# Optimization experiments

Hardware: AMD Instinct MI355X
Metric: run time of the kernel (lower is better)

## Reference

```python
import jax, jax.numpy as jnp
import numpy as np

N = 50000   # nodes per side
H = 256     # hidden_dim
E = 800000  # edges per metapath (avg degree 16)
XAVIER_STD = 0.088  # gain 1.414 * sqrt(2/(H+H))


def setup_inputs() -> dict:
    key = jax.random.key(0)
    ks = jax.random.split(key, 32)
    inp = {}
    inp["h_d"] = jax.random.normal(ks[0], (N, H), dtype=jnp.float32)
    inp["h_p"] = jax.random.normal(ks[1], (N, H), dtype=jnp.float32)
    i = 2
    for name in ["d0", "d1", "p0", "p1"]:
        inp[name + "_idx"] = jax.random.randint(ks[i], (2, E), 0, N, dtype=jnp.int32); i += 1
        inp[name + "_val"] = jax.random.uniform(ks[i], (E,), dtype=jnp.float32); i += 1
    # per-metapath GCN params: Linear weight [H,H] (no bias), additive bias [H], PReLU slope (scalar)
    for name in ["d0", "d1", "p0", "p1"]:
        inp["W" + name] = jax.random.normal(ks[i], (H, H), dtype=jnp.float32) * XAVIER_STD; i += 1
        inp["b" + name] = jnp.zeros((H,), jnp.float32)
        inp["a" + name] = jnp.full((1,), 0.25, jnp.float32)
    # per-side attention params: fc weight/bias, att vector [1,H]
    for s in ["d", "p"]:
        inp["fcW" + s] = jax.random.normal(ks[i], (H, H), dtype=jnp.float32) * XAVIER_STD; i += 1
        inp["fcb" + s] = jnp.zeros((H,), jnp.float32)
        inp["att" + s] = jax.random.normal(ks[i], (1, H), dtype=jnp.float32) * XAVIER_STD; i += 1
    return inp


def _gcn(h, W, b, a, idx, val):
    # Linear (no bias) -> sparse COO spmm -> bias -> PReLU
    fts = h @ W.T                                  # [N,H]
    msg = val[:, None] * fts[idx[1]]               # gather source rows [E,H]
    out = jax.ops.segment_sum(msg, idx[0], num_segments=h.shape[0]) + b
    return jnp.where(out > 0, out, a * out)        # PReLU, shared slope


def _attn_fuse(embeds, Wf, bf, att):
    # score_p = att . mean_n(tanh(fc(embed_p)))  -> softmax over metapaths
    sp = jnp.stack([jnp.tanh(e @ Wf.T + bf).mean(axis=0) for e in embeds])  # [P,H]
    beta = jax.nn.softmax(sp @ att[0])                                      # [P]
    return jnp.einsum('p,pnh->nh', beta, jnp.stack(embeds))


def reference(h_d, h_p, d0_idx, d0_val, d1_idx, d1_val, p0_idx, p0_val,
              p1_idx, p1_val, Wd0, bd0, ad0, Wd1, bd1, ad1,
              Wp0, bp0, ap0, Wp1, bp1, ap1,
              fcWd, fcbd, attd, fcWp, fcbp, attp):
    embeds_d = [_gcn(h_d, Wd0, bd0, ad0, d0_idx, d0_val),
                _gcn(h_d, Wd1, bd1, ad1, d1_idx, d1_val)]
    z_d = _attn_fuse(embeds_d, fcWd, fcbd, attd)
    embeds_p = [_gcn(h_p, Wp0, bp0, ap0, p0_idx, p0_val),
                _gcn(h_p, Wp1, bp1, ap1, p1_idx, p1_val)]
    z_p = _attn_fuse(embeds_p, fcWp, fcbp, attp)
    return (z_d, z_p)
```

## Files before the change

kernel.cpp:

```cpp
#include <hip/hip_runtime.h>
#include <cstdint>

#define H 256
#define NBMAX 400
#define CAPB 16

typedef unsigned short u16;
typedef __attribute__((ext_vector_type(8))) short short8;
typedef __attribute__((ext_vector_type(4))) float f32x4;

__device__ __forceinline__ float bf2f(u16 u) {
  return __uint_as_float(((unsigned)u) << 16);
}
__device__ __forceinline__ u16 f2bf(float f) {
  unsigned u = __float_as_uint(f);
  u = (u + 0x7FFF + ((u >> 16) & 1)) >> 16;
  return (u16)u;
}
__device__ __forceinline__ void async16(const void* g, void* l) {
  __builtin_amdgcn_global_load_lds((const __attribute__((address_space(1))) void*)g,
                                   (__attribute__((address_space(3))) void*)l, 16, 0, 0);
}

__global__ __launch_bounds__(256) void cvt_bf16(
    const float* __restrict__ h0, const float* __restrict__ h1,
    u16* __restrict__ dst, int total, size_t NH)
{
  const float* src = blockIdx.y ? h1 : h0;
  u16* d = dst + (size_t)blockIdx.y * NH;
  int i = (blockIdx.x * 256 + threadIdx.x) * 4;
  if (i >= total) return;
  float4 x = *(const float4*)(src + i);
  *(ushort4*)(d + i) = make_ushort4(f2bf(x.x), f2bf(x.y), f2bf(x.z), f2bf(x.w));
}

__global__ __launch_bounds__(256) void cvt_weights(
    const float* w0, const float* w1, const float* w2, const float* w3,
    const float* w4, const float* w5, u16* __restrict__ dst)
{
  const float* srcs[6] = {w0, w1, w2, w3, w4, w5};
  const float* s = srcs[blockIdx.y];
  int i = (blockIdx.x * 256 + threadIdx.x) * 4;
  float4 x = *(const float4*)(s + i);
  *(ushort4*)(dst + blockIdx.y * (H * H) + i) =
      make_ushort4(f2bf(x.x), f2bf(x.y), f2bf(x.z), f2bf(x.w));
}

__device__ __forceinline__ int block_incl_scan(int v) {
  __shared__ int wsum[4];
  int tid = threadIdx.x, lane = tid & 63, w = tid >> 6;
  int x = v;
  #pragma unroll
  for (int off = 1; off < 64; off <<= 1) {
    int n = __shfl_up(x, off);
    if (lane >= off) x += n;
  }
  if (lane == 63) wsum[w] = x;
  __syncthreads();
  int add = 0;
  #pragma unroll
  for (int i = 0; i < 4; ++i) add += (i < w) ? wsum[i] : 0;
  return x + add;
}

__global__ __launch_bounds__(1024) void hist_coarse(
    const int* i0, const int* i1, const int* i2, const int* i3,
    int* __restrict__ bcnt, int E, int nbuck)
{
  int mp = blockIdx.y;
  const int* idxs[4] = {i0, i1, i2, i3};
  const int* idx = idxs[mp];
  __shared__ int lh[NBMAX];
  int t = threadIdx.x;
  for (int i = t; i < nbuck; i += 1024) lh[i] = 0;
  __syncthreads();
  for (int e = blockIdx.x * 1024 + t; e < E; e += gridDim.x * 1024)
    atomicAdd(&lh[idx[e] >> 7], 1);
  __syncthreads();
  for (int i = t; i < nbuck; i += 1024) {
    int v = lh[i];
    if (v) atomicAdd(&bcnt[mp * nbuck + i], v);
  }
}

__global__ __launch_bounds__(256) void scan_buckets(
    const int* __restrict__ bcnt, int* __restrict__ bbase,
    int* __restrict__ gcur, int* __restrict__ rowptr, int N, int E, int nbuck)
{
  int mp = blockIdx.y;
  int t = threadIdx.x;
  int i0 = t * 2, i1 = t * 2 + 1;
  int a = (i0 < nbuck) ? bcnt[mp * nbuck + i0] : 0;
  int b = (i1 < nbuck) ? bcnt[mp * nbuck + i1] : 0;
  int s = a + b;
  int incl = block_incl_scan(s);
  int ex = incl - s;
  if (i0 < nbuck) { bbase[mp * nbuck + i0] = ex;     gcur[mp * nbuck + i0] = ex; }
  if (i1 < nbuck) { bbase[mp * nbuck + i1] = ex + a; gcur[mp * nbuck + i1] = ex + a; }
  if (t == 0) rowptr[mp * (N + 1) + N] = E;
}

__global__ __launch_bounds__(1024) void scatter_binned(
    const int* i0, const int* i1, const int* i2, const int* i3,
    const float* v0, const float* v1, const float* v2, const float* v3,
    int* __restrict__ gcur, int2* __restrict__ edgesB, int E, int nbuck)
{
  int mp = blockIdx.y;
  const int* idxs[4] = {i0, i1, i2, i3};
  const float* vals[4] = {v0, v1, v2, v3};
  const int* idx = idxs[mp];
  const float* val = vals[mp];
  int* cur = gcur + mp * nbuck;
  int2* out = edgesB + (size_t)mp * E;

  __shared__ int cnt[NBMAX];
  __shared__ int2 slab[NBMAX * CAPB];
  int t = threadIdx.x;
  for (int i = t; i < nbuck; i += 1024) cnt[i] = 0;
  __syncthreads();

  for (int base_e = blockIdx.x * 2048; base_e < E; base_e += gridDim.x * 2048) {
    #pragma unroll
    for (int u = 0; u < 2; ++u) {
      int e = base_e + u * 1024 + t;
      if (e < E) {
        int d = idx[e];
        int s = idx[E + e];
        float v = val[e];
        int bb = d >> 7;
        int2 pk = make_int2(s | ((d & 127) << 16), __float_as_int(v));
        int slot = atomicAdd(&cnt[bb], 1);
        if (slot < CAPB) slab[bb * CAPB + slot] = pk;
        else {
          int pos = atomicAdd(&cur[bb], 1);
          out[pos] = pk;
        }
      }
    }
    __syncthreads();
    for (int bb = t; bb < nbuck; bb += 1024) {
      int c = cnt[bb];
      if (c > CAPB) c = CAPB;
      if (c >= 8) {
        int ng = c >> 3;
        int pos = atomicAdd(&cur[bb], ng * 8);
        for (int k = 0; k < ng * 8; ++k) out[pos + k] = slab[bb * CAPB + k];
        int r = c & 7;
        for (int k = 0; k < r; ++k)
          slab[bb * CAPB + k] = slab[bb * CAPB + ng * 8 + k];
        cnt[bb] = r;
      }
    }
    __syncthreads();
  }
  for (int bb = t; bb < nbuck; bb += 1024) {
    int c = cnt[bb];
    if (c > CAPB) c = CAPB;
    if (c > 0) {
      int pos = atomicAdd(&cur[bb], c);
      for (int k = 0; k < c; ++k) out[pos + k] = slab[bb * CAPB + k];
    }
  }
}

__global__ __launch_bounds__(256) void bucket_to_csr(
    const int2* __restrict__ edgesB, const int* __restrict__ bbase,
    int* __restrict__ rowptr, int2* __restrict__ edges, int N, int E, int nbuck)
{
  int mp = blockIdx.y;
  int b = blockIdx.x;
  int base = bbase[mp * nbuck + b];
  int endp = (b + 1 < nbuck) ? bbase[mp * nbuck + b + 1] : E;
  int cntE = endp - base;
  const int2* in = edgesB + (size_t)mp * E + base;
  int2* out = edges + (size_t)mp * E;

  __shared__ int h[128], csum[128];
  int t = threadIdx.x;
  if (t < 128) h[t] = 0;
  __syncthreads();
  for (int k = t; k < cntE; k += 256)
    atomicAdd(&h[(in[k].x >> 16) & 127], 1);
  __syncthreads();
  if (t == 0) {
    int acc = 0;
    for (int i = 0; i < 128; ++i) { int c = h[i]; csum[i] = acc; acc += c; }
  }
  __syncthreads();
  int d0 = b << 7;
  if (t < 128 && d0 + t < N) rowptr[mp * (N + 1) + d0 + t] = base + csum[t];
  if (t < 128) h[t] = csum[t];
  __syncthreads();
  for (int k = t; k < cntE; k += 256) {
    int2 pk = in[k];
    int dl = (pk.x >> 16) & 127;
    int pos = atomicAdd(&h[dl], 1);
    out[base + pos] = make_int2(pk.x & 0xFFFF, pk.y);
  }
}

__global__ __launch_bounds__(256) void spmm_csr(
    const u16* __restrict__ hbf, const int* __restrict__ rowptrAll,
    const int2* __restrict__ edgesAll, u16* __restrict__ aggAll,
    int N, int E, size_t NH)
{
  int mp = blockIdx.y;
  const u16* fts = hbf + (size_t)(mp >> 1) * NH;
  const int* rowptr = rowptrAll + (size_t)mp * (N + 1);
  const int2* edges = edgesAll + (size_t)mp * E;
  u16* agg = aggAll + (size_t)mp * NH;

  int gw = (int)((blockIdx.x * 256 + threadIdx.x) >> 6);
  if (gw >= N) return;
  int lane = threadIdx.x & 63;
  int beg = rowptr[gw], end = rowptr[gw + 1];
  float a0 = 0.f, a1 = 0.f, a2 = 0.f, a3 = 0.f;
  for (int base = beg; base < end; base += 64) {
    int k = base + lane;
    int2 ev = make_int2(0, 0);
    if (k < end) ev = edges[k];
    int cnt = min(64, end - base);
    int j = 0;
    for (; j + 8 <= cnt; j += 8) {
      int sj[8]; float vj[8]; ushort4 r[8];
      #pragma unroll
      for (int u = 0; u < 8; ++u) {
        sj[u] = __shfl(ev.x, j + u);
        vj[u] = __uint_as_float((unsigned)__shfl(ev.y, j + u));
      }
      #pragma unroll
      for (int u = 0; u < 8; ++u)
        r[u] = *(const ushort4*)(fts + (size_t)sj[u] * H + lane * 4);
      #pragma unroll
      for (int u = 0; u < 8; ++u) {
        a0 += vj[u] * bf2f(r[u].x);
        a1 += vj[u] * bf2f(r[u].y);
        a2 += vj[u] * bf2f(r[u].z);
        a3 += vj[u] * bf2f(r[u].w);
      }
    }
    for (; j + 4 <= cnt; j += 4) {
      int sj[4]; float vj[4]; ushort4 r[4];
      #pragma unroll
      for (int u = 0; u < 4; ++u) {
        sj[u] = __shfl(ev.x, j + u);
        vj[u] = __uint_as_float((unsigned)__shfl(ev.y, j + u));
      }
      #pragma unroll
      for (int u = 0; u < 4; ++u)
        r[u] = *(const ushort4*)(fts + (size_t)sj[u] * H + lane * 4);
      #pragma unroll
      for (int u = 0; u < 4; ++u) {
        a0 += vj[u] * bf2f(r[u].x);
        a1 += vj[u] * bf2f(r[u].y);
        a2 += vj[u] * bf2f(r[u].z);
        a3 += vj[u] * bf2f(r[u].w);
      }
    }
    for (; j < cnt; ++j) {
      int sj = __shfl(ev.x, j);
      float vj = __uint_as_float((unsigned)__shfl(ev.y, j));
      ushort4 r = *(const ushort4*)(fts + (size_t)sj * H + lane * 4);
      a0 += vj * bf2f(r.x);
      a1 += vj * bf2f(r.y);
      a2 += vj * bf2f(r.z);
      a3 += vj * bf2f(r.w);
    }
  }
  int c = lane * 4;
  *(ushort4*)(agg + (size_t)gw * H + c) =
      make_ushort4(f2bf(a0), f2bf(a1), f2bf(a2), f2bf(a3));
}

template <int MODE>
__global__ __launch_bounds__(256) void gemm_bt(
    const u16* __restrict__ Abase, const u16* __restrict__ Wbase,
    u16* __restrict__ Cbase,
    const float* bp0, const float* bp1, const float* bp2, const float* bp3,
    const float* ap0, const float* ap1, const float* ap2, const float* ap3,
    float* __restrict__ colsum, int M, size_t NH)
{
  const int pi = blockIdx.z;
  const float* bps[4] = {bp0, bp1, bp2, bp3};
  const float* aps[4] = {ap0, ap1, ap2, ap3};
  const u16* A = Abase + (size_t)pi * NH;
  const u16* W;
  u16* C = nullptr;
  const float* bias;
  float* cs = nullptr;
  float al = 0.f;
  if (MODE == 0) {
    W = Wbase + (size_t)pi * (H * H);
    C = Cbase + (size_t)pi * NH;
    bias = bps[pi];
    al = aps[pi][0];
  } else {
    W = Wbase + (size_t)(pi >> 1) * (H * H);
    bias = (pi >> 1) ? bp1 : bp0;
    cs = colsum + (size_t)pi * H;
  }

  __shared__ u16 As[128 * 64];
  __shared__ u16 Bs[128 * 64];
  const int tid  = threadIdx.x;
  const int lane = tid & 63;
  const int wave = tid >> 6;
  const int quad = lane >> 4;
  const int l15  = lane & 15;
  const int m0 = blockIdx.x * 128;
  const int n0 = blockIdx.y * 128;
  const int wr = (wave & 1) * 64;
  const int wc = (wave >> 1) * 64;

  f32x4 acc[4][4] = {};

  for (int k0 = 0; k0 < H; k0 += 64) {
    #pragma unroll
    for (int r = 0; r < 4; ++r) {
      int chunk = r * 256 + tid;
      int row = chunk >> 3;
      int col = (chunk & 7) * 8;
      int gm = m0 + row; if (gm >= M) gm = M - 1;
      u16* lbase = As + (r * 256 + wave * 64) * 8;
      async16(A + (size_t)gm * H + k0 + col, lbase);
      u16* lbase2 = Bs + (r * 256 + wave * 64) * 8;
      async16(W + (size_t)(n0 + row) * H + k0 + col, lbase2);
    }
    __syncthreads();
    #pragma unroll
    for (int kk = 0; kk < 64; kk += 32) {
      short8 af[4], bf[4];
      #pragma unroll
      for (int i = 0; i < 4; ++i) {
        af[i] = *(const short8*)(As + (wr + i * 16 + l15) * 64 + kk + quad * 8);
        bf[i] = *(const short8*)(Bs + (wc + i * 16 + l15) * 64 + kk + quad * 8);
      }
      #pragma unroll
      for (int mi = 0; mi < 4; ++mi)
        #pragma unroll
        for (int ni = 0; ni < 4; ++ni)
          acc[mi][ni] = __builtin_amdgcn_mfma_f32_16x16x32_bf16(af[mi], bf[ni], acc[mi][ni], 0, 0, 0);
    }
    __syncthreads();
  }

  if (MODE == 0) {
    #pragma unroll
    for (int mi = 0; mi < 4; ++mi)
      #pragma unroll
      for (int ni = 0; ni < 4; ++ni) {
        int n = n0 + wc + ni * 16 + l15;
        float bv = bias[n];
        #pragma unroll
        for (int j = 0; j < 4; ++j) {
          int m = m0 + wr + mi * 16 + quad * 4 + j;
          if (m < M) {
            float x = acc[mi][ni][j] + bv;
            x = x > 0.f ? x : al * x;
            C[(size_t)m * H + n] = f2bf(x);
          }
        }
      }
  } else {
    #pragma unroll
    for (int ni = 0; ni < 4; ++ni) {
      int n = n0 + wc + ni * 16 + l15;
      float bv = bias[n];
      float s = 0.f;
      #pragma unroll
      for (int mi = 0; mi < 4; ++mi)
        #pragma unroll
        for (int j = 0; j < 4; ++j) {
          int m = m0 + wr + mi * 16 + quad * 4 + j;
          if (m < M) {
            float x = acc[mi][ni][j] + bv;
            s += 1.f - 2.f / (__expf(2.f * x) + 1.f);
          }
        }
      s += __shfl_xor(s, 16);
      s += __shfl_xor(s, 32);
      if (lane < 16) unsafeAtomicAdd(&cs[n], s);
    }
  }
}

__global__ __launch_bounds__(256) void compute_beta(
    const float* __restrict__ sp, const float* attd, const float* attp,
    float invN, float* __restrict__ beta)
{
  __shared__ float red0[4], red1[4];
  int s = blockIdx.y;
  const float* att = s ? attp : attd;
  const float* spb = sp + (size_t)(2 * s) * H;
  int t = threadIdx.x;
  float a = att[t];
  float s0 = spb[t] * invN * a;
  float s1 = spb[H + t] * invN * a;
  #pragma unroll
  for (int off = 32; off > 0; off >>= 1) {
    s0 += __shfl_down(s0, off);
    s1 += __shfl_down(s1, off);
  }
  int lane = t & 63, w = t >> 6;
  if (lane == 0) { red0[w] = s0; red1[w] = s1; }
  __syncthreads();
  if (t == 0) {
    float a0 = red0[0] + red0[1] + red0[2] + red0[3];
    float a1 = red1[0] + red1[1] + red1[2] + red1[3];
    float mx = fmaxf(a0, a1);
    float e0v = __expf(a0 - mx), e1v = __expf(a1 - mx);
    float inv = 1.f / (e0v + e1v);
    beta[2 * s]     = e0v * inv;
    beta[2 * s + 1] = e1v * inv;
  }
}

__global__ __launch_bounds__(256) void fuse_out(
    const u16* __restrict__ eAll, const float* __restrict__ beta,
    float* __restrict__ out, int total, size_t NH)
{
  int s = blockIdx.y;
  const u16* e0 = eAll + (size_t)(2 * s) * NH;
  const u16* e1 = eAll + (size_t)(2 * s + 1) * NH;
  float* o = out + (size_t)s * NH;
  int i = (blockIdx.x * 256 + threadIdx.x) * 4;
  if (i >= total) return;
  float b0 = beta[2 * s], b1 = beta[2 * s + 1];
  ushort4 u0 = *(const ushort4*)(e0 + i);
  ushort4 u1 = *(const ushort4*)(e1 + i);
  float4 ov;
  ov.x = b0 * bf2f(u0.x) + b1 * bf2f(u1.x);
  ov.y = b0 * bf2f(u0.y) + b1 * bf2f(u1.y);
  ov.z = b0 * bf2f(u0.z) + b1 * bf2f(u1.z);
  ov.w = b0 * bf2f(u0.w) + b1 * bf2f(u1.w);
  *(float4*)(o + i) = ov;
}

extern "C" void kernel_launch(void* const* d_in, const int* in_sizes, int n_in,
                              void* d_out, int out_size, void* d_ws, size_t ws_size,
                              hipStream_t stream)
{
  const float* h_in[2] = {(const float*)d_in[0], (const float*)d_in[1]};
  const int N = in_sizes[0] / H;
  const int E = in_sizes[3];
  const int* idx[4]; const float* val[4];
  for (int i = 0; i < 4; ++i) {
    idx[i] = (const int*)d_in[2 + 2 * i];
    val[i] = (const float*)d_in[3 + 2 * i];
  }
  const float *W[4], *bia[4], *alp[4];
  for (int i = 0; i < 4; ++i) {
    W[i]   = (const float*)d_in[10 + 3 * i];
    bia[i] = (const float*)d_in[11 + 3 * i];
    alp[i] = (const float*)d_in[12 + 3 * i];
  }
  const float *fcW[2], *fcb[2], *att[2];
  for (int s = 0; s < 2; ++s) {
    fcW[s] = (const float*)d_in[22 + 3 * s];
    fcb[s] = (const float*)d_in[23 + 3 * s];
    att[s] = (const float*)d_in[24 + 3 * s];
  }

  const size_t NH = (size_t)N * H;
  const int nbuck = (N + 127) >> 7;
  auto align256 = [](size_t x) { return (x + 255) & ~(size_t)255; };
  char* p = (char*)d_ws;
  u16* hbf = (u16*)p;      p += align256((size_t)2 * NH * 2);
  u16* aggAll = (u16*)p;   p += align256((size_t)4 * NH * 2);
  u16* eAll = (u16*)p;     p += align256((size_t)4 * NH * 2);
  u16* Wbf = (u16*)p;      p += align256((size_t)6 * H * H * 2);
  int* bcnt = (int*)p;     p += align256((size_t)4 * NBMAX * 4);
  int* bbase = (int*)p;    p += align256((size_t)4 * NBMAX * 4);
  int* gcur = (int*)p;     p += align256((size_t)4 * NBMAX * 4);
  int* rowptr = (int*)p;   p += align256((size_t)4 * (N + 1) * 4);
  int2* edges = (int2*)p;  p += align256((size_t)4 * E * 8);
  float* sp = (float*)p;   p += align256((size_t)4 * H * 4);
  float* beta = (float*)p;
  int2* edgesB = (int2*)aggAll;

  const int gx = (N + 127) / 128;
  const int tot = (int)NH;
  const int el_blocks = (tot / 4 + 255) / 256;
  const int spmm_blocks = (N + 3) / 4;

  dim3 wgrid(H * H / 1024, 6);
  cvt_weights<<<wgrid, 256, 0, stream>>>(W[0], W[1], W[2], W[3], fcW[0], fcW[1], Wbf);

  hipMemsetAsync(bcnt, 0, (size_t)4 * NBMAX * 4, stream);
  hipMemsetAsync(sp, 0, (size_t)4 * H * 4, stream);
  hist_coarse<<<dim3(64, 4), 1024, 0, stream>>>(idx[0], idx[1], idx[2], idx[3],
                                                bcnt, E, nbuck);
  scan_buckets<<<dim3(1, 4), 256, 0, stream>>>(bcnt, bbase, gcur, rowptr, N, E, nbuck);
  scatter_binned<<<dim3(64, 4), 1024, 0, stream>>>(idx[0], idx[1], idx[2], idx[3],
                                                   val[0], val[1], val[2], val[3],
                                                   gcur, edgesB, E, nbuck);
  bucket_to_csr<<<dim3(nbuck, 4), 256, 0, stream>>>(edgesB, bbase, rowptr, edges,
                                                    N, E, nbuck);

  cvt_bf16<<<dim3(el_blocks, 2), 256, 0, stream>>>(h_in[0], h_in[1], hbf, tot, NH);

  spmm_csr<<<dim3(spmm_blocks, 4), 256, 0, stream>>>(
      hbf, rowptr, edges, aggAll, N, E, NH);

  gemm_bt<0><<<dim3(gx, 2, 4), 256, 0, stream>>>(
      aggAll, Wbf, eAll,
      bia[0], bia[1], bia[2], bia[3],
      alp[0], alp[1], alp[2], alp[3],
      nullptr, N, NH);

  gemm_bt<1><<<dim3(gx, 2, 4), 256, 0, stream>>>(
      eAll, Wbf + (size_t)4 * H * H, nullptr,
      fcb[0], fcb[1], nullptr, nullptr,
      nullptr, nullptr, nullptr, nullptr,
      sp, N, NH);

  compute_beta<<<dim3(1, 2), 256, 0, stream>>>(sp, att[0], att[1],
                                               1.0f / (float)N, beta);

  fuse_out<<<dim3(el_blocks, 2), 256, 0, stream>>>(eAll, beta, (float*)d_out, tot, NH);
}
```

Before: 727.3 us.

## Widen GEMM tiles to full N=256 and fuse prep and beta kernels

```diff
diff --git a/kernel.cpp b/kernel.cpp
--- a/kernel.cpp
+++ b/kernel.cpp
@@ -22,28 +22,36 @@
                                    (__attribute__((address_space(3))) void*)l, 16, 0, 0);
 }
 
-__global__ __launch_bounds__(256) void cvt_bf16(
+__global__ __launch_bounds__(256) void prep(
     const float* __restrict__ h0, const float* __restrict__ h1,
-    u16* __restrict__ dst, int total, size_t NH)
-{
-  const float* src = blockIdx.y ? h1 : h0;
-  u16* d = dst + (size_t)blockIdx.y * NH;
-  int i = (blockIdx.x * 256 + threadIdx.x) * 4;
-  if (i >= total) return;
-  float4 x = *(const float4*)(src + i);
-  *(ushort4*)(d + i) = make_ushort4(f2bf(x.x), f2bf(x.y), f2bf(x.z), f2bf(x.w));
-}
-
-__global__ __launch_bounds__(256) void cvt_weights(
+    u16* __restrict__ hbf,
     const float* w0, const float* w1, const float* w2, const float* w3,
-    const float* w4, const float* w5, u16* __restrict__ dst)
-{
-  const float* srcs[6] = {w0, w1, w2, w3, w4, w5};
-  const float* s = srcs[blockIdx.y];
-  int i = (blockIdx.x * 256 + threadIdx.x) * 4;
-  float4 x = *(const float4*)(s + i);
-  *(ushort4*)(dst + blockIdx.y * (H * H) + i) =
-      make_ushort4(f2bf(x.x), f2bf(x.y), f2bf(x.z), f2bf(x.w));
+    const float* w4, const float* w5, u16* __restrict__ Wbf,
+    int* __restrict__ bcnt, float* __restrict__ sp, int total, size_t NH)
+{
+  int y = blockIdx.y;
+  int tid = threadIdx.x;
+  if (y < 2) {
+    const float* src = y ? h1 : h0;
+    u16* d = hbf + (size_t)y * NH;
+    int i = (blockIdx.x * 256 + tid) * 4;
+    if (i >= total) return;
+    float4 x = *(const float4*)(src + i);
+    *(ushort4*)(d + i) = make_ushort4(f2bf(x.x), f2bf(x.y), f2bf(x.z), f2bf(x.w));
+  } else {
+    int x = blockIdx.x;
+    if (x < 384) {
+      const float* srcs[6] = {w0, w1, w2, w3, w4, w5};
+      int m = x >> 6;
+      int i = ((x & 63) * 256 + tid) * 4;
+      float4 v = *(const float4*)(srcs[m] + i);
+      *(ushort4*)(Wbf + (size_t)m * (H * H) + i) =
+          make_ushort4(f2bf(v.x), f2bf(v.y), f2bf(v.z), f2bf(v.w));
+    } else if (x == 384) {
+      for (int i = tid; i < 4 * NBMAX; i += 256) bcnt[i] = 0;
+      for (int i = tid; i < 4 * H; i += 256) sp[i] = 0.f;
+    }
+  }
 }
 
 __device__ __forceinline__ int block_incl_scan(int v) {
@@ -301,18 +309,17 @@
   }
 
   __shared__ u16 As[128 * 64];
-  __shared__ u16 Bs[128 * 64];
+  __shared__ u16 Bs[256 * 64];
   const int tid  = threadIdx.x;
   const int lane = tid & 63;
   const int wave = tid >> 6;
   const int quad = lane >> 4;
   const int l15  = lane & 15;
   const int m0 = blockIdx.x * 128;
-  const int n0 = blockIdx.y * 128;
   const int wr = (wave & 1) * 64;
-  const int wc = (wave >> 1) * 64;
-
-  f32x4 acc[4][4] = {};
+  const int wc = (wave >> 1) * 128;
+
+  f32x4 acc[4][8] = {};
 
   for (int k0 = 0; k0 < H; k0 += 64) {
     #pragma unroll
@@ -321,24 +328,29 @@
       int row = chunk >> 3;
       int col = (chunk & 7) * 8;
       int gm = m0 + row; if (gm >= M) gm = M - 1;
-      u16* lbase = As + (r * 256 + wave * 64) * 8;
-      async16(A + (size_t)gm * H + k0 + col, lbase);
-      u16* lbase2 = Bs + (r * 256 + wave * 64) * 8;
-      async16(W + (size_t)(n0 + row) * H + k0 + col, lbase2);
+      async16(A + (size_t)gm * H + k0 + col, As + (r * 256 + wave * 64) * 8);
+    }
+    #pragma unroll
+    for (int r = 0; r < 8; ++r) {
+      int chunk = r * 256 + tid;
+      int row = chunk >> 3;
+      int col = (chunk & 7) * 8;
+      async16(W + (size_t)row * H + k0 + col, Bs + (r * 256 + wave * 64) * 8);
     }
     __syncthreads();
     #pragma unroll
     for (int kk = 0; kk < 64; kk += 32) {
-      short8 af[4], bf[4];
-      #pragma unroll
-      for (int i = 0; i < 4; ++i) {
+      short8 af[4], bf[8];
+      #pragma unroll
+      for (int i = 0; i < 4; ++i)
         af[i] = *(const short8*)(As + (wr + i * 16 + l15) * 64 + kk + quad * 8);
+      #pragma unroll
+      for (int i = 0; i < 8; ++i)
         bf[i] = *(const short8*)(Bs + (wc + i * 16 + l15) * 64 + kk + quad * 8);
-      }
       #pragma unroll
       for (int mi = 0; mi < 4; ++mi)
         #pragma unroll
-        for (int ni = 0; ni < 4; ++ni)
+        for (int ni = 0; ni < 8; ++ni)
           acc[mi][ni] = __builtin_amdgcn_mfma_f32_16x16x32_bf16(af[mi], bf[ni], acc[mi][ni], 0, 0, 0);
     }
     __syncthreads();
@@ -348,8 +360,8 @@
     #pragma unroll
     for (int mi = 0; mi < 4; ++mi)
       #pragma unroll
-      for (int ni = 0; ni < 4; ++ni) {
-        int n = n0 + wc + ni * 16 + l15;
+      for (int ni = 0; ni < 8; ++ni) {
+        int n = wc + ni * 16 + l15;
         float bv = bias[n];
         #pragma unroll
         for (int j = 0; j < 4; ++j) {
@@ -363,8 +375,8 @@
       }
   } else {
     #pragma unroll
-    for (int ni = 0; ni < 4; ++ni) {
-      int n = n0 + wc + ni * 16 + l15;
+    for (int ni = 0; ni < 8; ++ni) {
+      int n = wc + ni * 16 + l15;
       float bv = bias[n];
       float s = 0.f;
       #pragma unroll
@@ -384,15 +396,17 @@
   }
 }
 
-__global__ __launch_bounds__(256) void compute_beta(
-    const float* __restrict__ sp, const float* attd, const float* attp,
-    float invN, float* __restrict__ beta)
+__global__ __launch_bounds__(256) void fuse_out(
+    const u16* __restrict__ eAll, const float* __restrict__ sp,
+    const float* attd, const float* attp, float invN,
+    float* __restrict__ out, int total, size_t NH)
 {
   __shared__ float red0[4], red1[4];
+  __shared__ float sb0, sb1;
   int s = blockIdx.y;
+  int t = threadIdx.x;
   const float* att = s ? attp : attd;
   const float* spb = sp + (size_t)(2 * s) * H;
-  int t = threadIdx.x;
   float a = att[t];
   float s0 = spb[t] * invN * a;
   float s1 = spb[H + t] * invN * a;
@@ -410,22 +424,17 @@
     float mx = fmaxf(a0, a1);
     float e0v = __expf(a0 - mx), e1v = __expf(a1 - mx);
     float inv = 1.f / (e0v + e1v);
-    beta[2 * s]     = e0v * inv;
-    beta[2 * s + 1] = e1v * inv;
-  }
-}
-
-__global__ __launch_bounds__(256) void fuse_out(
-    const u16* __restrict__ eAll, const float* __restrict__ beta,
-    float* __restrict__ out, int total, size_t NH)
-{
-  int s = blockIdx.y;
+    sb0 = e0v * inv;
+    sb1 = e1v * inv;
+  }
+  __syncthreads();
+  float b0 = sb0, b1 = sb1;
+
   const u16* e0 = eAll + (size_t)(2 * s) * NH;
   const u16* e1 = eAll + (size_t)(2 * s + 1) * NH;
   float* o = out + (size_t)s * NH;
-  int i = (blockIdx.x * 256 + threadIdx.x) * 4;
+  int i = (blockIdx.x * 256 + t) * 4;
   if (i >= total) return;
-  float b0 = beta[2 * s], b1 = beta[2 * s + 1];
   ushort4 u0 = *(const ushort4*)(e0 + i);
   ushort4 u1 = *(const ushort4*)(e1 + i);
   float4 ov;
@@ -474,8 +483,7 @@
   int* gcur = (int*)p;     p += align256((size_t)4 * NBMAX * 4);
   int* rowptr = (int*)p;   p += align256((size_t)4 * (N + 1) * 4);
   int2* edges = (int2*)p;  p += align256((size_t)4 * E * 8);
-  float* sp = (float*)p;   p += align256((size_t)4 * H * 4);
-  float* beta = (float*)p;
+  float* sp = (float*)p;
   int2* edgesB = (int2*)aggAll;
 
   const int gx = (N + 127) / 128;
@@ -483,11 +491,11 @@
   const int el_blocks = (tot / 4 + 255) / 256;
   const int spmm_blocks = (N + 3) / 4;
 
-  dim3 wgrid(H * H / 1024, 6);
-  cvt_weights<<<wgrid, 256, 0, stream>>>(W[0], W[1], W[2], W[3], fcW[0], fcW[1], Wbf);
-
-  hipMemsetAsync(bcnt, 0, (size_t)4 * NBMAX * 4, stream);
-  hipMemsetAsync(sp, 0, (size_t)4 * H * 4, stream);
+  prep<<<dim3(el_blocks, 3), 256, 0, stream>>>(
+      h_in[0], h_in[1], hbf,
+      W[0], W[1], W[2], W[3], fcW[0], fcW[1], Wbf,
+      bcnt, sp, tot, NH);
+
   hist_coarse<<<dim3(64, 4), 1024, 0, stream>>>(idx[0], idx[1], idx[2], idx[3],
                                                 bcnt, E, nbuck);
   scan_buckets<<<dim3(1, 4), 256, 0, stream>>>(bcnt, bbase, gcur, rowptr, N, E, nbuck);
@@ -497,25 +505,21 @@
   bucket_to_csr<<<dim3(nbuck, 4), 256, 0, stream>>>(edgesB, bbase, rowptr, edges,
                                                     N, E, nbuck);
 
-  cvt_bf16<<<dim3(el_blocks, 2), 256, 0, stream>>>(h_in[0], h_in[1], hbf, tot, NH);
-
   spmm_csr<<<dim3(spmm_blocks, 4), 256, 0, stream>>>(
       hbf, rowptr, edges, aggAll, N, E, NH);
 
-  gemm_bt<0><<<dim3(gx, 2, 4), 256, 0, stream>>>(
+  gemm_bt<0><<<dim3(gx, 1, 4), 256, 0, stream>>>(
       aggAll, Wbf, eAll,
       bia[0], bia[1], bia[2], bia[3],
       alp[0], alp[1], alp[2], alp[3],
       nullptr, N, NH);
 
-  gemm_bt<1><<<dim3(gx, 2, 4), 256, 0, stream>>>(
+  gemm_bt<1><<<dim3(gx, 1, 4), 256, 0, stream>>>(
       eAll, Wbf + (size_t)4 * H * H, nullptr,
       fcb[0], fcb[1], nullptr, nullptr,
       nullptr, nullptr, nullptr, nullptr,
       sp, N, NH);
 
-  compute_beta<<<dim3(1, 2), 256, 0, stream>>>(sp, att[0], att[1],
-                                               1.0f / (float)N, beta);
-
-  fuse_out<<<dim3(el_blocks, 2), 256, 0, stream>>>(eAll, beta, (float*)d_out, tot, NH);
-}
+  fuse_out<<<dim3(el_blocks, 2), 256, 0, stream>>>(
+      eAll, sp, att[0], att[1], 1.0f / (float)N, (float*)d_out, tot, NH);
+}
```

Result: slower. 870.1 us (+19.6%).
